# Optimization experiments

Hardware: AMD Instinct MI355X
Metric: run time of the kernel (lower is better)

## Reference

```python
import jax, jax.numpy as jnp
import numpy as np

BS, NWP, D, NEXP, H, OUT = 32768, 10, 256, 6, 64, 2

def setup_inputs() -> dict:
    key = jax.random.key(0)
    ks = jax.random.split(key, 8)
    x = jax.random.normal(ks[0], (BS, NWP, D), dtype=jnp.float32)
    measurements = jax.random.randint(ks[1], (BS, 1), 0, NEXP, dtype=jnp.int32)
    rank_embed = 0.02 * jax.random.normal(ks[2], (1, NWP, D), dtype=jnp.float32)
    # Linear weights stored as [in, out] for einsum; biases [out]
    W1 = 0.05 * jax.random.normal(ks[3], (NEXP, D, H), dtype=jnp.float32)
    b1 = 0.05 * jax.random.normal(ks[4], (NEXP, H), dtype=jnp.float32)
    W2 = 0.05 * jax.random.normal(ks[5], (NEXP, H, OUT), dtype=jnp.float32)
    b2 = 0.05 * jax.random.normal(ks[6], (NEXP, OUT), dtype=jnp.float32)
    return {"x": x, "measurements": measurements, "rank_embed": rank_embed,
            "W1": W1, "b1": b1, "W2": W2, "b2": b2}

def reference(x, measurements, rank_embed, W1, b1, W2, b2):
    command = measurements[:, 0]                      # [bs] int in [0,6)
    xr = x + rank_embed                               # [bs, 10, d]
    # Dense 6-way expert MLP (matches original: all heads computed for all samples)
    h = jax.nn.relu(jnp.einsum('bnd,edh->benh', xr, W1) + b1[None, :, None, :])  # [bs,6,10,64]
    wp = jnp.einsum('benh,eho->beno', h, W2) + b2[None, :, None, :]              # [bs,6,10,2]
    sel = jnp.take_along_axis(wp, command[:, None, None, None].astype(jnp.int32), axis=1)[:, 0]  # [bs,10,2]
    return jnp.cumsum(sel, axis=1)
```

## Files before the change

kernel.cpp:

```cpp
#include <hip/hip_runtime.h>
#include <hip/hip_bf16.h>

#define BS 32768
#define NWP 10
#define DD 256
#define NEXP 6
#define HH 64
#define OUT_DIM 2
#define MB 32
#define MAXQ 1032

typedef short bf16x8 __attribute__((ext_vector_type(8)));
typedef float f32x4 __attribute__((ext_vector_type(4)));

__device__ inline short bfs(float f) {
  __hip_bfloat16 h = __float2bfloat16(f);
  return __builtin_bit_cast(short, h);
}

__global__ __launch_bounds__(1024) void aux_k(const int* __restrict__ cmd,
                                              const float* __restrict__ W1,
                                              const float* __restrict__ re,
                                              const float* __restrict__ b1,
                                              int* __restrict__ counts,
                                              int* __restrict__ lists,
                                              short* __restrict__ W1T,
                                              float* __restrict__ rw) {
  const int bid = blockIdx.x;
  const int tid = threadIdx.x;

  if (bid < 32) {
    __shared__ int wcnt[16][NEXP];
    __shared__ int wbase[16][NEXP];
    const int w = tid >> 6, lane = tid & 63;
    const int b = bid * 1024 + tid;
    const int e = cmd[b];
    #pragma unroll
    for (int ee = 0; ee < NEXP; ++ee) {
      unsigned long long m = __ballot(e == ee);
      if (lane == 0) wcnt[w][ee] = __popcll(m);
    }
    __syncthreads();
    if (tid < NEXP) {
      int tot = 0, pf[16];
      #pragma unroll
      for (int ww = 0; ww < 16; ++ww) { pf[ww] = tot; tot += wcnt[ww][tid]; }
      const int bb = atomicAdd(&counts[tid], tot);
      #pragma unroll
      for (int ww = 0; ww < 16; ++ww) wbase[ww][tid] = bb + pf[ww];
    }
    __syncthreads();
    #pragma unroll
    for (int ee = 0; ee < NEXP; ++ee) {
      unsigned long long m = __ballot(e == ee);
      if (e == ee) {
        const int nbelow = __popcll(m & ((1ull << lane) - 1ull));
        lists[ee * BS + wbase[w][ee] + nbelow] = b;
      }
    }
  } else if (bid < 44) {
    const int e = (bid - 32) >> 1;
    const int h = ((bid - 32) & 1) * 32 + (tid >> 5);
    const int d0 = (tid & 31) * 8;
    const float* wp = W1 + (size_t)e * DD * HH + h;
    bf16x8 v;
    #pragma unroll
    for (int i = 0; i < 8; ++i) v[i] = bfs(wp[(size_t)(d0 + i) * HH]);
    *(bf16x8*)(W1T + ((size_t)e * HH + h) * DD + d0) = v;
  } else {
    const int e = bid - 44;
    if (tid < NWP * HH) {
      const int n = tid >> 6, h = tid & 63;
      const float* rp = re + (size_t)n * DD;
      const float* wp = W1 + (size_t)e * DD * HH + h;
      float s = b1[e * HH + h];
      for (int d = 0; d < DD; ++d) s += rp[d] * wp[(size_t)d * HH];
      rw[((size_t)e * NWP + n) * HH + h] = s;
    }
  }
}

__global__ __launch_bounds__(256, 2) void moe_gemm_k(
    const float* __restrict__ x,
    const short* __restrict__ W1T,
    const float* __restrict__ rwg,
    const float* __restrict__ W2,
    const float* __restrict__ b2,
    const int* __restrict__ qmeta,
    const int* __restrict__ lists,
    float* __restrict__ out)
{
  __shared__ short Xa[4][16 * DD];
  __shared__ float rwl[NWP][68];
  __shared__ float w2l[HH * OUT_DIM];
  __shared__ float po[MB * NWP][2];

  const int wi = blockIdx.x;
  int acc0 = 0, e = -1, start = 0;
  #pragma unroll
  for (int ee = 0; ee < NEXP; ++ee) {
    const int nc = (qmeta[ee] + MB - 1) >> 5;
    if (e < 0 && wi < acc0 + nc) { e = ee; start = (wi - acc0) * MB; }
    acc0 += nc;
  }
  if (e < 0) return;
  const int cnt = qmeta[e];
  const int nb = min(MB, cnt - start);
  const int nrows = nb * NWP;

  const int tid = threadIdx.x;
  const int lane = tid & 63;
  const int wv = tid >> 6;
  const int arow = lane & 15;
  const int ag = lane >> 4;
  const int lbase = e * BS + start;

  bf16x8 Wf[4][8];
  {
    const short* wb = W1T + ((size_t)e * HH + arow) * DD + ag * 8;
    #pragma unroll
    for (int nt = 0; nt < 4; ++nt)
      #pragma unroll
      for (int ks = 0; ks < 8; ++ks)
        Wf[nt][ks] = *(const bf16x8*)(wb + (size_t)(nt * 16) * DD + ks * 32);
  }
  for (int i = tid; i < NWP * HH; i += 256)
    rwl[i >> 6][i & 63] = rwg[(size_t)e * NWP * HH + i];
  if (tid < HH * OUT_DIM) w2l[tid] = W2[(size_t)e * HH * OUT_DIM + tid];

  __syncthreads();

  short* Xw = &Xa[wv][0];
  const int ntile = (nrows + 15) >> 4;

  for (int t = wv; t < ntile; t += 4) {
    #pragma unroll
    for (int r = 0; r < 16; ++r) {
      const int rowu = __builtin_amdgcn_readfirstlane(min(t * 16 + r, nrows - 1));
      const int item = rowu / NWP;
      const int nn = rowu - item * NWP;
      const int gb = lists[lbase + item];
      const f32x4 xv = __builtin_nontemporal_load(
          (const f32x4*)(x + ((size_t)gb * NWP + nn) * DD + lane * 4));
      short4 pk = make_short4(bfs(xv[0]), bfs(xv[1]), bfs(xv[2]), bfs(xv[3]));
      *(short4*)&Xw[r * DD + ((lane * 4) ^ ((r & 7) << 3))] = pk;
    }

    f32x4 acc[4] = {{0,0,0,0},{0,0,0,0},{0,0,0,0},{0,0,0,0}};
    #pragma unroll
    for (int ks = 0; ks < 8; ++ks) {
      const int kidx = ks * 32 + ag * 8;
      const bf16x8 bx = *(const bf16x8*)&Xw[arow * DD + (kidx ^ ((arow & 7) << 3))];
      #pragma unroll
      for (int nt = 0; nt < 4; ++nt)
        acc[nt] = __builtin_amdgcn_mfma_f32_16x16x32_bf16(Wf[nt][ks], bx, acc[nt], 0, 0, 0);
    }

    const int row = t * 16 + arow;
    const int rowc = min(row, nrows - 1);
    const int nn = rowc - (rowc / NWP) * NWP;
    float p0 = 0.f, p1 = 0.f;
    #pragma unroll
    for (int nt = 0; nt < 4; ++nt) {
      const int h0 = nt * 16 + ag * 4;
      const float4 rv = *(const float4*)&rwl[nn][h0];
      const float4 wa = *(const float4*)&w2l[h0 * 2];
      const float4 wb = *(const float4*)&w2l[h0 * 2 + 4];
      const float h0v = fmaxf(acc[nt][0] + rv.x, 0.f);
      const float h1v = fmaxf(acc[nt][1] + rv.y, 0.f);
      const float h2v = fmaxf(acc[nt][2] + rv.z, 0.f);
      const float h3v = fmaxf(acc[nt][3] + rv.w, 0.f);
      p0 += h0v * wa.x + h1v * wa.z + h2v * wb.x + h3v * wb.z;
      p1 += h0v * wa.y + h1v * wa.w + h2v * wb.y + h3v * wb.w;
    }
    p0 += __shfl_xor(p0, 16); p1 += __shfl_xor(p1, 16);
    p0 += __shfl_xor(p0, 32); p1 += __shfl_xor(p1, 32);
    if (ag == 0 && row < nrows) {
      po[row][0] = p0;
      po[row][1] = p1;
    }
  }

  __syncthreads();

  if (tid < nb) {
    const int gb = lists[lbase + tid];
    const float bb0 = b2[e * OUT_DIM + 0];
    const float bb1 = b2[e * OUT_DIM + 1];
    float v[NWP * OUT_DIM];
    float s0 = 0.f, s1 = 0.f;
    #pragma unroll
    for (int n = 0; n < NWP; ++n) {
      s0 += po[tid * NWP + n][0] + bb0;
      s1 += po[tid * NWP + n][1] + bb1;
      v[n * 2 + 0] = s0;
      v[n * 2 + 1] = s1;
    }
    float4* op = (float4*)(out + (size_t)gb * NWP * OUT_DIM);
    #pragma unroll
    for (int q = 0; q < 5; ++q)
      op[q] = make_float4(v[q * 4], v[q * 4 + 1], v[q * 4 + 2], v[q * 4 + 3]);
  }
}

extern "C" void kernel_launch(void* const* d_in, const int* in_sizes, int n_in,
                              void* d_out, int out_size, void* d_ws, size_t ws_size,
                              hipStream_t stream) {
  const float* x          = (const float*)d_in[0];
  const int*   meas       = (const int*)d_in[1];
  const float* rank_embed = (const float*)d_in[2];
  const float* W1         = (const float*)d_in[3];
  const float* b1         = (const float*)d_in[4];
  const float* W2         = (const float*)d_in[5];
  const float* b2         = (const float*)d_in[6];
  float* out = (float*)d_out;

  int* qmeta = (int*)d_ws;
  int* lists = (int*)((char*)d_ws + 8192);
  short* W1T = (short*)((char*)d_ws + (800 << 10));
  float* rw  = (float*)((char*)d_ws + (1000 << 10));

  hipMemsetAsync(d_ws, 0, 256, stream);
  aux_k<<<50, 1024, 0, stream>>>(meas, W1, rank_embed, b1, qmeta, lists, W1T, rw);
  moe_gemm_k<<<MAXQ, 256, 0, stream>>>(x, W1T, rw, W2, b2, qmeta, lists, out);
}
```

Before: 101.1 us.

## Replace global expert bucketing with per-block local sort of 8 items

Drops the global expert-bucketing pass (memset, atomics, index lists). Each block now takes 8 consecutive items, sorts them by expert in shared memory, and runs MFMA over runs of same-expert rows, with each wave owning 16 hidden units and reading W1T from global per run. This removes a launch and the indirect gather through lists, and raises occupancy to 3 blocks per SM. The cost is that weights are reloaded per run with no reuse across many items, row tiles that straddle runs are computed redundantly, and rw and W2 are read from global inside the loop.

```diff
diff --git a/kernel.cpp b/kernel.cpp
--- a/kernel.cpp
+++ b/kernel.cpp
@@ -7,8 +7,8 @@
 #define NEXP 6
 #define HH 64
 #define OUT_DIM 2
-#define MB 32
-#define MAXQ 1032
+#define IB 8
+#define RPB (IB * NWP)
 
 typedef short bf16x8 __attribute__((ext_vector_type(8)));
 typedef float f32x4 __attribute__((ext_vector_type(4)));
@@ -18,49 +18,16 @@
   return __builtin_bit_cast(short, h);
 }
 
-__global__ __launch_bounds__(1024) void aux_k(const int* __restrict__ cmd,
-                                              const float* __restrict__ W1,
+__global__ __launch_bounds__(1024) void aux_k(const float* __restrict__ W1,
                                               const float* __restrict__ re,
                                               const float* __restrict__ b1,
-                                              int* __restrict__ counts,
-                                              int* __restrict__ lists,
                                               short* __restrict__ W1T,
                                               float* __restrict__ rw) {
   const int bid = blockIdx.x;
   const int tid = threadIdx.x;
-
-  if (bid < 32) {
-    __shared__ int wcnt[16][NEXP];
-    __shared__ int wbase[16][NEXP];
-    const int w = tid >> 6, lane = tid & 63;
-    const int b = bid * 1024 + tid;
-    const int e = cmd[b];
-    #pragma unroll
-    for (int ee = 0; ee < NEXP; ++ee) {
-      unsigned long long m = __ballot(e == ee);
-      if (lane == 0) wcnt[w][ee] = __popcll(m);
-    }
-    __syncthreads();
-    if (tid < NEXP) {
-      int tot = 0, pf[16];
-      #pragma unroll
-      for (int ww = 0; ww < 16; ++ww) { pf[ww] = tot; tot += wcnt[ww][tid]; }
-      const int bb = atomicAdd(&counts[tid], tot);
-      #pragma unroll
-      for (int ww = 0; ww < 16; ++ww) wbase[ww][tid] = bb + pf[ww];
-    }
-    __syncthreads();
-    #pragma unroll
-    for (int ee = 0; ee < NEXP; ++ee) {
-      unsigned long long m = __ballot(e == ee);
-      if (e == ee) {
-        const int nbelow = __popcll(m & ((1ull << lane) - 1ull));
-        lists[ee * BS + wbase[w][ee] + nbelow] = b;
-      }
-    }
-  } else if (bid < 44) {
-    const int e = (bid - 32) >> 1;
-    const int h = ((bid - 32) & 1) * 32 + (tid >> 5);
+  if (bid < 12) {
+    const int e = bid >> 1;
+    const int h = (bid & 1) * 32 + (tid >> 5);
     const int d0 = (tid & 31) * 8;
     const float* wp = W1 + (size_t)e * DD * HH + h;
     bf16x8 v;
@@ -68,7 +35,7 @@
     for (int i = 0; i < 8; ++i) v[i] = bfs(wp[(size_t)(d0 + i) * HH]);
     *(bf16x8*)(W1T + ((size_t)e * HH + h) * DD + d0) = v;
   } else {
-    const int e = bid - 44;
+    const int e = bid - 12;
     if (tid < NWP * HH) {
       const int n = tid >> 6, h = tid & 63;
       const float* rp = re + (size_t)n * DD;
@@ -80,123 +47,130 @@
   }
 }
 
-__global__ __launch_bounds__(256, 2) void moe_gemm_k(
+__global__ __launch_bounds__(256, 3) void moe_gemm_k(
     const float* __restrict__ x,
+    const int* __restrict__ cmd,
     const short* __restrict__ W1T,
     const float* __restrict__ rwg,
     const float* __restrict__ W2,
     const float* __restrict__ b2,
-    const int* __restrict__ qmeta,
-    const int* __restrict__ lists,
     float* __restrict__ out)
 {
-  __shared__ short Xa[4][16 * DD];
-  __shared__ float rwl[NWP][68];
-  __shared__ float w2l[HH * OUT_DIM];
-  __shared__ float po[MB * NWP][2];
+  __shared__ short Xb[RPB * DD];
+  __shared__ float po[RPB][4][2];
+  __shared__ int pm[IB];
+  __shared__ int se[IB];
+  __shared__ int rb[IB + 1];
+  __shared__ int eg[IB];
+  __shared__ int nrun_s;
+  __shared__ int eload[IB];
 
-  const int wi = blockIdx.x;
-  int acc0 = 0, e = -1, start = 0;
-  #pragma unroll
-  for (int ee = 0; ee < NEXP; ++ee) {
-    const int nc = (qmeta[ee] + MB - 1) >> 5;
-    if (e < 0 && wi < acc0 + nc) { e = ee; start = (wi - acc0) * MB; }
-    acc0 += nc;
-  }
-  if (e < 0) return;
-  const int cnt = qmeta[e];
-  const int nb = min(MB, cnt - start);
-  const int nrows = nb * NWP;
-
+  const int b0 = blockIdx.x * IB;
   const int tid = threadIdx.x;
   const int lane = tid & 63;
   const int wv = tid >> 6;
   const int arow = lane & 15;
   const int ag = lane >> 4;
-  const int lbase = e * BS + start;
 
-  bf16x8 Wf[4][8];
-  {
-    const short* wb = W1T + ((size_t)e * HH + arow) * DD + ag * 8;
-    #pragma unroll
-    for (int nt = 0; nt < 4; ++nt)
-      #pragma unroll
-      for (int ks = 0; ks < 8; ++ks)
-        Wf[nt][ks] = *(const bf16x8*)(wb + (size_t)(nt * 16) * DD + ks * 32);
-  }
-  for (int i = tid; i < NWP * HH; i += 256)
-    rwl[i >> 6][i & 63] = rwg[(size_t)e * NWP * HH + i];
-  if (tid < HH * OUT_DIM) w2l[tid] = W2[(size_t)e * HH * OUT_DIM + tid];
-
+  if (tid < IB) eload[tid] = cmd[b0 + tid];
   __syncthreads();
 
-  short* Xw = &Xa[wv][0];
-  const int ntile = (nrows + 15) >> 4;
+  if (tid == 0) {
+    int ei[IB], id[IB];
+    #pragma unroll
+    for (int i = 0; i < IB; ++i) { ei[i] = eload[i]; id[i] = i; }
+    #pragma unroll
+    for (int i = 1; i < IB; ++i) {
+      const int ev = ei[i], iv = id[i];
+      int j = i - 1;
+      while (j >= 0 && ei[j] > ev) { ei[j+1] = ei[j]; id[j+1] = id[j]; --j; }
+      ei[j+1] = ev; id[j+1] = iv;
+    }
+    int nr = 0;
+    #pragma unroll
+    for (int i = 0; i < IB; ++i) {
+      pm[i] = id[i]; se[i] = ei[i];
+      if (i == 0 || ei[i] != ei[i-1]) { rb[nr] = i * NWP; eg[nr] = ei[i]; ++nr; }
+    }
+    rb[nr] = RPB;
+    nrun_s = nr;
+  }
+  __syncthreads();
 
-  for (int t = wv; t < ntile; t += 4) {
+  {
+    const int g0 = b0 + pm[wv * 2];
+    const int g1 = b0 + pm[wv * 2 + 1];
     #pragma unroll
-    for (int r = 0; r < 16; ++r) {
-      const int rowu = __builtin_amdgcn_readfirstlane(min(t * 16 + r, nrows - 1));
-      const int item = rowu / NWP;
-      const int nn = rowu - item * NWP;
-      const int gb = lists[lbase + item];
+    for (int i = 0; i < 20; ++i) {
+      const int gitem = (i < 10) ? g0 : g1;
+      const int n = (i < 10) ? i : i - 10;
+      const int s = wv * 20 + i;
       const f32x4 xv = __builtin_nontemporal_load(
-          (const f32x4*)(x + ((size_t)gb * NWP + nn) * DD + lane * 4));
+          (const f32x4*)(x + ((size_t)gitem * NWP + n) * DD + lane * 4));
       short4 pk = make_short4(bfs(xv[0]), bfs(xv[1]), bfs(xv[2]), bfs(xv[3]));
-      *(short4*)&Xw[r * DD + ((lane * 4) ^ ((r & 7) << 3))] = pk;
+      *(short4*)&Xb[s * DD + ((lane * 4) ^ ((s & 7) << 3))] = pk;
     }
+  }
+  __syncthreads();
 
-    f32x4 acc[4] = {{0,0,0,0},{0,0,0,0},{0,0,0,0},{0,0,0,0}};
+  const int nrun = nrun_s;
+  for (int g = 0; g < nrun; ++g) {
+    const int r0 = rb[g], r1 = rb[g + 1];
+    const int e = eg[g];
+    const short* wq = W1T + ((size_t)e * HH + wv * 16 + arow) * DD + ag * 8;
+    bf16x8 Wq[8];
     #pragma unroll
-    for (int ks = 0; ks < 8; ++ks) {
-      const int kidx = ks * 32 + ag * 8;
-      const bf16x8 bx = *(const bf16x8*)&Xw[arow * DD + (kidx ^ ((arow & 7) << 3))];
+    for (int ks = 0; ks < 8; ++ks) Wq[ks] = *(const bf16x8*)(wq + ks * 32);
+    const int h0 = wv * 16 + ag * 4;
+    const float4 wa = *(const float4*)(W2 + ((size_t)e * HH + h0) * OUT_DIM);
+    const float4 wb = *(const float4*)(W2 + ((size_t)e * HH + h0 + 2) * OUT_DIM);
+
+    const int t0 = r0 >> 4, t1 = (r1 - 1) >> 4;
+    for (int t = t0; t <= t1; ++t) {
+      const int row = t * 16 + arow;
+      f32x4 acc = {0.f, 0.f, 0.f, 0.f};
       #pragma unroll
-      for (int nt = 0; nt < 4; ++nt)
-        acc[nt] = __builtin_amdgcn_mfma_f32_16x16x32_bf16(Wf[nt][ks], bx, acc[nt], 0, 0, 0);
-    }
-
-    const int row = t * 16 + arow;
-    const int rowc = min(row, nrows - 1);
-    const int nn = rowc - (rowc / NWP) * NWP;
-    float p0 = 0.f, p1 = 0.f;
-    #pragma unroll
-    for (int nt = 0; nt < 4; ++nt) {
-      const int h0 = nt * 16 + ag * 4;
-      const float4 rv = *(const float4*)&rwl[nn][h0];
-      const float4 wa = *(const float4*)&w2l[h0 * 2];
-      const float4 wb = *(const float4*)&w2l[h0 * 2 + 4];
-      const float h0v = fmaxf(acc[nt][0] + rv.x, 0.f);
-      const float h1v = fmaxf(acc[nt][1] + rv.y, 0.f);
-      const float h2v = fmaxf(acc[nt][2] + rv.z, 0.f);
-      const float h3v = fmaxf(acc[nt][3] + rv.w, 0.f);
-      p0 += h0v * wa.x + h1v * wa.z + h2v * wb.x + h3v * wb.z;
-      p1 += h0v * wa.y + h1v * wa.w + h2v * wb.y + h3v * wb.w;
-    }
-    p0 += __shfl_xor(p0, 16); p1 += __shfl_xor(p1, 16);
-    p0 += __shfl_xor(p0, 32); p1 += __shfl_xor(p1, 32);
-    if (ag == 0 && row < nrows) {
-      po[row][0] = p0;
-      po[row][1] = p1;
+      for (int ks = 0; ks < 8; ++ks) {
+        const int kidx = ks * 32 + ag * 8;
+        const bf16x8 bx = *(const bf16x8*)&Xb[row * DD + (kidx ^ ((arow & 7) << 3))];
+        acc = __builtin_amdgcn_mfma_f32_16x16x32_bf16(Wq[ks], bx, acc, 0, 0, 0);
+      }
+      const int n = row - (row / NWP) * NWP;
+      const float4 rv = *(const float4*)(rwg + ((size_t)e * NWP + n) * HH + h0);
+      const float h0v = fmaxf(acc[0] + rv.x, 0.f);
+      const float h1v = fmaxf(acc[1] + rv.y, 0.f);
+      const float h2v = fmaxf(acc[2] + rv.z, 0.f);
+      const float h3v = fmaxf(acc[3] + rv.w, 0.f);
+      float p0 = h0v * wa.x + h1v * wa.z + h2v * wb.x + h3v * wb.z;
+      float p1 = h0v * wa.y + h1v * wa.w + h2v * wb.y + h3v * wb.w;
+      p0 += __shfl_xor(p0, 16); p1 += __shfl_xor(p1, 16);
+      p0 += __shfl_xor(p0, 32); p1 += __shfl_xor(p1, 32);
+      if (ag == 0 && row >= r0 && row < r1) {
+        po[row][wv][0] = p0;
+        po[row][wv][1] = p1;
+      }
     }
   }
 
   __syncthreads();
 
-  if (tid < nb) {
-    const int gb = lists[lbase + tid];
+  if (tid < IB) {
+    const int j = tid;
+    const int gitem = b0 + pm[j];
+    const int e = se[j];
     const float bb0 = b2[e * OUT_DIM + 0];
     const float bb1 = b2[e * OUT_DIM + 1];
     float v[NWP * OUT_DIM];
     float s0 = 0.f, s1 = 0.f;
     #pragma unroll
     for (int n = 0; n < NWP; ++n) {
-      s0 += po[tid * NWP + n][0] + bb0;
-      s1 += po[tid * NWP + n][1] + bb1;
+      const int row = j * NWP + n;
+      s0 += po[row][0][0] + po[row][1][0] + po[row][2][0] + po[row][3][0] + bb0;
+      s1 += po[row][0][1] + po[row][1][1] + po[row][2][1] + po[row][3][1] + bb1;
       v[n * 2 + 0] = s0;
       v[n * 2 + 1] = s1;
     }
-    float4* op = (float4*)(out + (size_t)gb * NWP * OUT_DIM);
+    float4* op = (float4*)(out + (size_t)gitem * NWP * OUT_DIM);
     #pragma unroll
     for (int q = 0; q < 5; ++q)
       op[q] = make_float4(v[q * 4], v[q * 4 + 1], v[q * 4 + 2], v[q * 4 + 3]);
@@ -215,12 +189,9 @@
   const float* b2         = (const float*)d_in[6];
   float* out = (float*)d_out;
 
-  int* qmeta = (int*)d_ws;
-  int* lists = (int*)((char*)d_ws + 8192);
-  short* W1T = (short*)((char*)d_ws + (800 << 10));
-  float* rw  = (float*)((char*)d_ws + (1000 << 10));
+  short* W1T = (short*)d_ws;
+  float* rw  = (float*)((char*)d_ws + (256 << 10));
 
-  hipMemsetAsync(d_ws, 0, 256, stream);
-  aux_k<<<50, 1024, 0, stream>>>(meas, W1, rank_embed, b1, qmeta, lists, W1T, rw);
-  moe_gemm_k<<<MAXQ, 256, 0, stream>>>(x, W1T, rw, W2, b2, qmeta, lists, out);
+  aux_k<<<18, 1024, 0, stream>>>(W1, rank_embed, b1, W1T, rw);
+  moe_gemm_k<<<BS / IB, 256, 0, stream>>>(x, meas, W1T, rw, W2, b2, out);
 }
```

Result: slower. 143.7 us (+42.1%).
